# Performance work log

Hardware: AMD Instinct MI355X
Metric: run time of the kernel (lower is better)

## Reference

```python
import jax, jax.numpy as jnp
import numpy as np

H, NH, QLORA, KVLORA, DN, DR, DV = 2048, 16, 1536, 512, 128, 64, 128
QD = DN + DR  # 192
EPS = 1e-6
ROPE_BASE = 10000.0


def rmsnorm(x, g):
    var = jnp.mean(x * x, axis=-1, keepdims=True)
    return x * jax.lax.rsqrt(var + EPS) * g


def rotate_half(x):
    x1, x2 = jnp.split(x, 2, axis=-1)
    return jnp.concatenate([-x2, x1], axis=-1)


def rope_cos_sin(seq_len):
    inv_freq = 1.0 / (ROPE_BASE ** (jnp.arange(0, DR, 2, dtype=jnp.float32) / DR))
    t = jnp.arange(seq_len, dtype=jnp.float32)
    freqs = jnp.outer(t, inv_freq)           # [S, DR/2]
    emb = jnp.concatenate([freqs, freqs], -1)  # [S, DR]
    return jnp.cos(emb), jnp.sin(emb)


def setup_inputs() -> dict:
    key = jax.random.key(0)
    ks = jax.random.split(key, 6)
    B, S = 2, 2048
    sc = 0.02
    return {
        "hidden_states": jax.random.normal(ks[0], (B, S, H), jnp.float32),
        "w_qa": jax.random.normal(ks[1], (QLORA, H), jnp.float32) * sc,
        "g_qa": jnp.ones((QLORA,), jnp.float32),
        "w_qb": jax.random.normal(ks[2], (NH * QD, QLORA), jnp.float32) * sc,
        "w_kva": jax.random.normal(ks[3], (KVLORA + DR, H), jnp.float32) * sc,
        "g_kva": jnp.ones((KVLORA,), jnp.float32),
        "w_kvb": jax.random.normal(ks[4], (NH * (DN + DV), KVLORA), jnp.float32) * sc,
        "w_o": jax.random.normal(ks[5], (H, NH * DV), jnp.float32) * sc,
    }


def reference(hidden_states, w_qa, g_qa, w_qb, w_kva, g_kva, w_kvb, w_o):
    B, S, _ = hidden_states.shape
    # Q path: low-rank down-proj -> RMSNorm -> up-proj
    q_a = hidden_states @ w_qa.T                        # [B,S,QLORA]
    q = rmsnorm(q_a, g_qa) @ w_qb.T                     # [B,S,NH*QD]
    q = q.reshape(B, S, NH, QD).transpose(0, 2, 1, 3)   # [B,NH,S,QD]
    q_nope, q_pe = q[..., :DN], q[..., DN:]
    # KV path: joint down-proj with MQA rope slice
    ckv = hidden_states @ w_kva.T                       # [B,S,KVLORA+DR]
    compressed_kv, k_pe = ckv[..., :KVLORA], ckv[..., KVLORA:]
    k_pe = k_pe.reshape(B, S, 1, DR).transpose(0, 2, 1, 3)  # [B,1,S,DR]
    kv = rmsnorm(compressed_kv, g_kva) @ w_kvb.T        # [B,S,NH*(DN+DV)]
    kv = kv.reshape(B, S, NH, DN + DV).transpose(0, 2, 1, 3)
    k_nope, v = kv[..., :DN], kv[..., DN:]              # [B,NH,S,DN], [B,NH,S,DV]
    # decoupled RoPE on rope sub-dims only
    cos, sin = rope_cos_sin(S)                          # [S,DR]
    cos = cos[None, None]; sin = sin[None, None]
    q_pe = q_pe * cos + rotate_half(q_pe) * sin
    k_pe = k_pe * cos + rotate_half(k_pe) * sin
    query = jnp.concatenate([q_nope, q_pe], -1)         # [B,NH,S,QD]
    key = jnp.concatenate([k_nope, jnp.broadcast_to(k_pe, (B, NH, S, DR))], -1)
    # causal SDPA with scale = QD**-0.5
    scale = QD ** (-0.5)
    scores = jnp.einsum("bhsd,bhtd->bhst", query, key) * scale
    mask = jnp.tril(jnp.ones((S, S), bool))
    scores = jnp.where(mask, scores, jnp.finfo(scores.dtype).min)
    attn = jax.nn.softmax(scores, axis=-1)
    out = jnp.einsum("bhst,bhtd->bhsd", attn, v)        # [B,NH,S,DV]
    out = out.transpose(0, 2, 1, 3).reshape(B, S, NH * DV)
    return out @ w_o.T
```

## Files before the change

kernel.cpp:

```cpp
#include <hip/hip_runtime.h>
#include <cstdint>
#include <cstring>

typedef short short8 __attribute__((ext_vector_type(8)));
typedef float float4v __attribute__((ext_vector_type(4)));
typedef float float4g __attribute__((ext_vector_type(4)));
typedef unsigned short ushort4v __attribute__((ext_vector_type(4)));
typedef unsigned int uint2v __attribute__((ext_vector_type(2)));

typedef __attribute__((address_space(3))) unsigned int lds_uint;
typedef __attribute__((address_space(1))) const unsigned int glob_uint;

static __device__ __forceinline__ void async16(void* lds, const void* g) {
    __builtin_amdgcn_global_load_lds((glob_uint*)g, (lds_uint*)lds, 16, 0, 0);
}

static __device__ __forceinline__ float b2f(unsigned short u) {
    unsigned int x = ((unsigned int)u) << 16;
    float f;
    __builtin_memcpy(&f, &x, 4);
    return f;
}
static __device__ __forceinline__ unsigned short f2b(float f) {
    unsigned int x;
    __builtin_memcpy(&x, &f, 4);
    unsigned int r = (x + 0x7fffu + ((x >> 16) & 1u)) >> 16;
    return (unsigned short)r;
}

__global__ __launch_bounds__(256) void k_f2b6(
    const float* __restrict__ s0, unsigned short* __restrict__ d0,
    const float* __restrict__ s1, unsigned short* __restrict__ d1,
    const float* __restrict__ s2, unsigned short* __restrict__ d2,
    const float* __restrict__ s3, unsigned short* __restrict__ d3,
    const float* __restrict__ s4, unsigned short* __restrict__ d4,
    const float* __restrict__ s5, unsigned short* __restrict__ d5,
    float qs) {
    int blk = blockIdx.x;
    const float* s; unsigned short* d; float sc = 1.f; int rel;
    if (blk < 8192)       { s = s0; d = d0; rel = blk; }
    else if (blk < 11264) { s = s1; d = d1; rel = blk - 8192; }
    else if (blk < 15872) { s = s2; d = d2; rel = blk - 11264; sc = qs; }
    else if (blk < 17024) { s = s3; d = d3; rel = blk - 15872; }
    else if (blk < 19072) { s = s4; d = d4; rel = blk - 17024; }
    else                  { s = s5; d = d5; rel = blk - 19072; }
    int i = (rel * 256 + threadIdx.x) * 4;
    float4g v = *(const float4g*)(s + i);
    ushort4v r;
    r.x = f2b(v.x * sc); r.y = f2b(v.y * sc); r.z = f2b(v.z * sc); r.w = f2b(v.w * sc);
    *(ushort4v*)(d + i) = r;
}

static __device__ __forceinline__ void gemm_bt_body(
    const unsigned short* __restrict__ A, int lda,
    const unsigned short* __restrict__ W,
    void* __restrict__ C, int ldc,
    int N, int K, int mode, int bx, int by,
    unsigned short* __restrict__ VT) {
    __shared__ __align__(16) unsigned short As[128 * 32];
    __shared__ __align__(16) unsigned short Ws[128 * 32];
    const int tid = threadIdx.x;
    const int m0 = by * 128, n0 = bx * 128;
    const int wave = tid >> 6, lane = tid & 63;
    const int wm = (wave >> 1) * 64, wn = (wave & 1) * 64;
    const int lrow = lane & 15, quad = lane >> 4;
    const int srow = lane >> 2, spiece = lane & 3;

    float4v acc[4][4];
    float4v z = {0.f, 0.f, 0.f, 0.f};
#pragma unroll
    for (int i = 0; i < 4; i++)
#pragma unroll
        for (int j = 0; j < 4; j++) acc[i][j] = z;

    for (int k0 = 0; k0 < K; k0 += 32) {
#pragma unroll
        for (int ii = 0; ii < 2; ++ii) {
            int i = wave + ii * 4;
            int row = i * 16 + srow;
            async16(&As[i * 512], &A[(size_t)(m0 + row) * lda + k0 + spiece * 8]);
            int wr = n0 + row;
            if (wr > N - 1) wr = N - 1;
            async16(&Ws[i * 512], &W[(size_t)wr * K + k0 + spiece * 8]);
        }
        __syncthreads();
        short8 af[4], bfr[4];
#pragma unroll
        for (int i = 0; i < 4; i++)
            af[i] = *(const short8*)&As[(wm + i * 16 + lrow) * 32 + quad * 8];
#pragma unroll
        for (int i = 0; i < 4; i++)
            bfr[i] = *(const short8*)&Ws[(wn + i * 16 + lrow) * 32 + quad * 8];
#pragma unroll
        for (int i = 0; i < 4; i++)
#pragma unroll
            for (int j = 0; j < 4; j++)
                acc[i][j] = __builtin_amdgcn_mfma_f32_16x16x32_bf16(af[i], bfr[j], acc[i][j], 0, 0, 0);
        __syncthreads();
    }

    const int rbase = quad * 4;
#pragma unroll
    for (int i = 0; i < 4; i++) {
#pragma unroll
        for (int j = 0; j < 4; j++) {
            int col = n0 + wn + j * 16 + lrow;
            if (col >= N) continue;
            if (mode == 2) {
                int dd = col & 255, h = col >> 8;
                int row0 = m0 + wm + i * 16 + rbase;
                if (dd < 128) {
#pragma unroll
                    for (int r = 0; r < 4; r++)
                        ((unsigned short*)C)[(size_t)(row0 + r) * ldc + col] = f2b(acc[i][j][r]);
                } else {
                    int b = row0 >> 11, s0 = row0 & 2047;
                    ushort4v pv;
                    pv.x = f2b(acc[i][j][0]); pv.y = f2b(acc[i][j][1]);
                    pv.z = f2b(acc[i][j][2]); pv.w = f2b(acc[i][j][3]);
                    *(ushort4v*)&VT[((size_t)(b * 16 + h) * 128 + (dd - 128)) * 2048 + s0] = pv;
                }
            } else {
#pragma unroll
                for (int r = 0; r < 4; r++) {
                    int row = m0 + wm + i * 16 + rbase + r;
                    float v = acc[i][j][r];
                    if (mode == 1)
                        ((float*)C)[(size_t)row * ldc + col] = v;
                    else
                        ((unsigned short*)C)[(size_t)row * ldc + col] = f2b(v);
                }
            }
        }
    }
}

__global__ __launch_bounds__(256, 3)
void k_gemm_bt(const unsigned short* __restrict__ A, int lda,
               const unsigned short* __restrict__ W,
               void* __restrict__ C, int ldc,
               int N, int K, int mode) {
    gemm_bt_body(A, lda, W, C, ldc, N, K, mode, blockIdx.x, blockIdx.y, nullptr);
}

__global__ __launch_bounds__(256, 3)
void k_gemm_dual(const unsigned short* __restrict__ A0, int lda0,
                 const unsigned short* __restrict__ W0, void* __restrict__ C0,
                 int ldc0, int N0, int K0, int nbx0,
                 const unsigned short* __restrict__ A1, int lda1,
                 const unsigned short* __restrict__ W1, void* __restrict__ C1,
                 int ldc1, int N1, int K1, int mode1,
                 unsigned short* __restrict__ VT) {
    int bx = blockIdx.x;
    if (bx < nbx0) {
        gemm_bt_body(A0, lda0, W0, C0, ldc0, N0, K0, 0, bx, blockIdx.y, nullptr);
    } else {
        gemm_bt_body(A1, lda1, W1, C1, ldc1, N1, K1, mode1, bx - nbx0, blockIdx.y, VT);
    }
}

__global__ __launch_bounds__(192) void k_norm2(
    unsigned short* __restrict__ qa, const float* __restrict__ g_qa,
    unsigned short* __restrict__ ckv, const float* __restrict__ g_kva) {
    __shared__ float wsum[3];
    int blk = blockIdx.x;
    int tid = threadIdx.x;
    if (blk < 4096) {
        size_t base = (size_t)blk * 1536 + tid * 8;
        short8 v8 = *(const short8*)(qa + base);
        float vf[8];
        float ss = 0.f;
#pragma unroll
        for (int i = 0; i < 8; i++) {
            vf[i] = b2f((unsigned short)v8[i]);
            ss += vf[i] * vf[i];
        }
        for (int off = 32; off > 0; off >>= 1) ss += __shfl_xor(ss, off);
        int wave = tid >> 6, lane = tid & 63;
        if (lane == 0) wsum[wave] = ss;
        __syncthreads();
        ss = wsum[0] + wsum[1] + wsum[2];
        float scale = rsqrtf(ss * (1.f / 1536.f) + 1e-6f);
        short8 r8;
#pragma unroll
        for (int i = 0; i < 8; i++) r8[i] = (short)f2b(vf[i] * scale * g_qa[tid * 8 + i]);
        *(short8*)(qa + base) = r8;
    } else {
        int row = blk - 4096;
        if (tid < 64) {
            size_t base = (size_t)row * 576 + tid * 8;
            short8 v8 = *(const short8*)(ckv + base);
            float vf[8];
            float ss = 0.f;
#pragma unroll
            for (int i = 0; i < 8; i++) {
                vf[i] = b2f((unsigned short)v8[i]);
                ss += vf[i] * vf[i];
            }
            for (int off = 32; off > 0; off >>= 1) ss += __shfl_xor(ss, off);
            float scale = rsqrtf(ss * (1.f / 512.f) + 1e-6f);
            short8 r8;
#pragma unroll
            for (int i = 0; i < 8; i++) r8[i] = (short)f2b(vf[i] * scale * g_kva[tid * 8 + i]);
            *(short8*)(ckv + base) = r8;
        } else if (tid < 96) {
            int d = tid - 64;
            int s = row & 2047;
            size_t base = (size_t)row * 576 + 512;
            float inv = exp2f((float)d * -0.4152410118609203f);
            float f = (float)s * inv;
            float c, sn;
            sincosf(f, &sn, &c);
            float x1 = b2f(ckv[base + d]), x2 = b2f(ckv[base + d + 32]);
            ckv[base + d] = f2b(x1 * c - x2 * sn);
            ckv[base + d + 32] = f2b(x2 * c + x1 * sn);
        }
    }
}

__global__ __launch_bounds__(256, 2)
void k_attn11(const unsigned short* __restrict__ q,
              const unsigned short* __restrict__ kv,
              const unsigned short* __restrict__ ckv,
              const unsigned short* __restrict__ vt,
              unsigned short* __restrict__ ao)
{
    __shared__ __align__(16) unsigned short Ks[2][12288];
    __shared__ __align__(16) unsigned short Vs[8192];
    __shared__ __align__(16) unsigned short Pl[4][1280];

    const int lb = blockIdx.x;
    const int qt = (lb < 256) ? (lb >> 5) : 15 - ((lb & 255) >> 5);
    const int bh = lb & 31;
    const int b = bh >> 4, h = bh & 15;
    const int tid = threadIdx.x, wave = tid >> 6, lane = tid & 63;
    const int lrow = lane & 15, quad = lane >> 4;
    const int srow = lane >> 2, spiece = lane & 3;
    const int tok0 = b * 2048 + qt * 128;
    unsigned short* Pw = Pl[wave];

    const int colx = spiece ^ ((srow >> 1) & 3);
    const int qx = (quad ^ ((lrow >> 1) & 3)) * 8;

    short8 qf[2][6];
#pragma unroll
    for (int mi = 0; mi < 2; mi++) {
        int row = wave * 32 + mi * 16 + lrow;
        const unsigned short* qp = q + (size_t)(tok0 + row) * 3072 + h * 192;
#pragma unroll
        for (int ks = 0; ks < 6; ks++) qf[mi][ks] = *(const short8*)(qp + ks * 32 + quad * 8);
        float sp = (float)(qt * 128 + row);
#pragma unroll
        for (int j = 0; j < 8; j++) {
            float inv = exp2f((float)(quad * 8 + j) * -0.4152410118609203f);
            float f = sp * inv;
            float c, sn;
            sincosf(f, &sn, &c);
            float x1 = b2f((unsigned short)qf[mi][4][j]);
            float x2 = b2f((unsigned short)qf[mi][5][j]);
            qf[mi][4][j] = (short)f2b(x1 * c - x2 * sn);
            qf[mi][5][j] = (short)f2b(x2 * c + x1 * sn);
        }
    }

    short8 ones;
#pragma unroll
    for (int j = 0; j < 8; j++) ones[j] = (short)0x3F80;

    float m_st[2];
    m_st[0] = m_st[1] = -__builtin_inff();
    float4v z4 = {0.f, 0.f, 0.f, 0.f};
    float4v o[2][8], osum[2];
#pragma unroll
    for (int mi = 0; mi < 2; mi++) {
        osum[mi] = z4;
#pragma unroll
        for (int dt = 0; dt < 8; dt++) o[mi][dt] = z4;
    }

    const int nk = 2 * qt + 2;

    auto stageK = [&](int kt, int buf) {
        const int kb = kt * 64;
#pragma unroll
        for (int ii = 0; ii < 6; ++ii) {
            int id = wave * 6 + ii;
            int ks = id >> 2;
            int row = (id & 3) * 16 + srow;
            int key = b * 2048 + kb + row;
            const unsigned short* g =
                (ks < 4) ? kv + (size_t)key * 4096 + h * 256 + ks * 32 + colx * 8
                         : ckv + (size_t)key * 576 + 512 + (ks - 4) * 32 + colx * 8;
            async16(&Ks[buf][id * 512], g);
        }
    };
    auto stageV = [&](int kt) {
        const int kb = kt * 64;
#pragma unroll
        for (int ii = 0; ii < 4; ++ii) {
            int id = wave * 4 + ii;
            int d = (id & 7) * 16 + srow;
            const unsigned short* g =
                vt + ((size_t)bh * 128 + d) * 2048 + kb + (id >> 3) * 32 + colx * 8;
            async16(&Vs[id * 512], g);
        }
    };

    stageK(0, 0);

    for (int kt = 0; kt < nk; ++kt) {
        __syncthreads();
        stageV(kt);
        if (kt + 1 < nk) stageK(kt + 1, (kt + 1) & 1);
        const unsigned short* Kb = Ks[kt & 1];
        const int kb = kt * 64;

        float4v sc[2][4];
#pragma unroll
        for (int mi = 0; mi < 2; mi++)
#pragma unroll
            for (int nt = 0; nt < 4; nt++) sc[mi][nt] = z4;
        __builtin_amdgcn_s_setprio(1);
#pragma unroll
        for (int ks = 0; ks < 6; ks++) {
#pragma unroll
            for (int nt = 0; nt < 4; nt++) {
                short8 kf = *(const short8*)&Kb[ks * 2048 + nt * 512 + lrow * 32 + qx];
                sc[0][nt] = __builtin_amdgcn_mfma_f32_16x16x32_bf16(kf, qf[0][ks], sc[0][nt], 0, 0, 0);
                sc[1][nt] = __builtin_amdgcn_mfma_f32_16x16x32_bf16(kf, qf[1][ks], sc[1][nt], 0, 0, 0);
            }
        }
        __builtin_amdgcn_s_setprio(0);

        if (kt >= nk - 2) {
#pragma unroll
            for (int mi = 0; mi < 2; mi++) {
                int rowc = qt * 128 + wave * 32 + mi * 16 + lrow;
#pragma unroll
                for (int nt = 0; nt < 4; nt++)
#pragma unroll
                    for (int r = 0; r < 4; r++) {
                        int keyc = kb + nt * 16 + quad * 4 + r;
                        if (keyc > rowc) sc[mi][nt][r] = -__builtin_inff();
                    }
            }
        }

        float mx[2];
#pragma unroll
        for (int mi = 0; mi < 2; mi++) {
            float m = sc[mi][0][0];
#pragma unroll
            for (int nt = 0; nt < 4; nt++)
#pragma unroll
                for (int r = 0; r < 4; r++) m = fmaxf(m, sc[mi][nt][r]);
            m = fmaxf(m, __shfl_xor(m, 16));
            m = fmaxf(m, __shfl_xor(m, 32));
            mx[mi] = m;
        }
        bool within = (mx[0] <= m_st[0] + 6.f) && (mx[1] <= m_st[1] + 6.f);
        if (!__all(within)) {
            float alpha[2];
#pragma unroll
            for (int mi = 0; mi < 2; mi++) {
                float mnew = fmaxf(m_st[mi], mx[mi]);
                alpha[mi] = exp2f(m_st[mi] - mnew);
                m_st[mi] = mnew;
            }
            float arow[2][4];
#pragma unroll
            for (int mi = 0; mi < 2; mi++)
#pragma unroll
                for (int r = 0; r < 4; r++) arow[mi][r] = __shfl(alpha[mi], quad * 4 + r);
#pragma unroll
            for (int mi = 0; mi < 2; mi++) {
#pragma unroll
                for (int r = 0; r < 4; r++) osum[mi][r] *= arow[mi][r];
#pragma unroll
                for (int dt = 0; dt < 8; dt++)
#pragma unroll
                    for (int r = 0; r < 4; r++) o[mi][dt][r] *= arow[mi][r];
            }
        }
        uint2v pk[2][4];
#pragma unroll
        for (int mi = 0; mi < 2; mi++) {
#pragma unroll
            for (int nt = 0; nt < 4; nt++) {
                float p0 = exp2f(sc[mi][nt][0] - m_st[mi]);
                float p1 = exp2f(sc[mi][nt][1] - m_st[mi]);
                float p2 = exp2f(sc[mi][nt][2] - m_st[mi]);
                float p3 = exp2f(sc[mi][nt][3] - m_st[mi]);
                pk[mi][nt].x = (unsigned int)f2b(p0) | ((unsigned int)f2b(p1) << 16);
                pk[mi][nt].y = (unsigned int)f2b(p2) | ((unsigned int)f2b(p3) << 16);
            }
        }

        __syncthreads();

#pragma unroll
        for (int ks2 = 0; ks2 < 2; ks2++) {
#pragma unroll
            for (int mi = 0; mi < 2; mi++) {
                int row = mi * 16 + lrow;
                *(uint2v*)&Pw[row * 40 + quad * 4] = pk[mi][ks2 * 2];
                *(uint2v*)&Pw[row * 40 + 16 + quad * 4] = pk[mi][ks2 * 2 + 1];
            }
            short8 pa0 = *(const short8*)&Pw[lrow * 40 + quad * 8];
            short8 pa1 = *(const short8*)&Pw[(16 + lrow) * 40 + quad * 8];
            __builtin_amdgcn_s_setprio(1);
#pragma unroll
            for (int dt = 0; dt < 8; dt++) {
                short8 vf = *(const short8*)&Vs[(ks2 * 8 + dt) * 512 + lrow * 32 + qx];
                o[0][dt] = __builtin_amdgcn_mfma_f32_16x16x32_bf16(pa0, vf, o[0][dt], 0, 0, 0);
                o[1][dt] = __builtin_amdgcn_mfma_f32_16x16x32_bf16(pa1, vf, o[1][dt], 0, 0, 0);
            }
            osum[0] = __builtin_amdgcn_mfma_f32_16x16x32_bf16(pa0, ones, osum[0], 0, 0, 0);
            osum[1] = __builtin_amdgcn_mfma_f32_16x16x32_bf16(pa1, ones, osum[1], 0, 0, 0);
            __builtin_amdgcn_s_setprio(0);
        }
    }

#pragma unroll
    for (int mi = 0; mi < 2; mi++) {
#pragma unroll
        for (int r = 0; r < 4; r++) {
            float linv = 1.f / osum[mi][r];
            unsigned short* dst =
                ao + (size_t)(tok0 + wave * 32 + mi * 16 + quad * 4 + r) * 2048 + h * 128;
#pragma unroll
            for (int dt = 0; dt < 8; dt++) dst[dt * 16 + lrow] = f2b(o[mi][dt][r] * linv);
        }
    }
}

extern "C" void kernel_launch(void* const* d_in, const int* in_sizes, int n_in,
                              void* d_out, int out_size, void* d_ws, size_t ws_size,
                              hipStream_t stream) {
    (void)in_sizes; (void)n_in; (void)out_size; (void)ws_size;
    const float* hs    = (const float*)d_in[0];
    const float* w_qa  = (const float*)d_in[1];
    const float* g_qa  = (const float*)d_in[2];
    const float* w_qb  = (const float*)d_in[3];
    const float* w_kva = (const float*)d_in[4];
    const float* g_kva = (const float*)d_in[5];
    const float* w_kvb = (const float*)d_in[6];
    const float* w_o   = (const float*)d_in[7];

    char* ws = (char*)d_ws;
    size_t off = 0;
    auto alloc = [&](size_t bytes) -> unsigned short* {
        unsigned short* p = (unsigned short*)(ws + off);
        off += (bytes + 255) & ~(size_t)255;
        return p;
    };
    unsigned short* hb    = alloc(4096ull * 2048 * 2);
    unsigned short* wqa   = alloc(1536ull * 2048 * 2);
    unsigned short* wqb   = alloc(3072ull * 1536 * 2);
    unsigned short* wkva  = alloc(576ull * 2048 * 2);
    unsigned short* wkvb  = alloc(4096ull * 512 * 2);
    unsigned short* wo    = alloc(2048ull * 2048 * 2);
    unsigned short* qa    = alloc(4096ull * 1536 * 2);
    unsigned short* ckv   = alloc(4096ull * 576 * 2);
    unsigned short* qbuf  = alloc(4096ull * 3072 * 2);
    unsigned short* kvbuf = alloc(4096ull * 4096 * 2);
    unsigned short* vtb   = alloc(32ull * 128 * 2048 * 2);
    unsigned short* ao    = alloc(4096ull * 2048 * 2);

    const float qscale = 0.07216878364870323f * 1.4426950408889634f;

    k_f2b6<<<dim3(23168), dim3(256), 0, stream>>>(
        hs, hb, w_qa, wqa, w_qb, wqb, w_kva, wkva, w_kvb, wkvb, w_o, wo, qscale);

    k_gemm_dual<<<dim3(17, 32), 256, 0, stream>>>(
        hb, 2048, wqa, qa, 1536, 1536, 2048, 12,
        hb, 2048, wkva, ckv, 576, 576, 2048, 0, nullptr);

    k_norm2<<<dim3(8192), dim3(192), 0, stream>>>(qa, g_qa, ckv, g_kva);

    k_gemm_dual<<<dim3(56, 32), 256, 0, stream>>>(
        qa, 1536, wqb, qbuf, 3072, 3072, 1536, 24,
        ckv, 576, wkvb, kvbuf, 4096, 4096, 512, 2, vtb);

    k_attn11<<<dim3(512), 256, 0, stream>>>(qbuf, kvbuf, ckv, vtb, ao);
    k_gemm_bt<<<dim3(16, 32), 256, 0, stream>>>(ao, 2048, wo, d_out, 2048, 2048, 2048, 1);
}
```

Measured before the change: 432.6 us.

## Triple-buffer GEMM LDS tiles with async prefetch two stages ahead

Replaces the single-buffered LDS tile loop in the shared GEMM body with a 3-stage ring buffer. Global-to-LDS async loads for tile t+2 are issued before the MFMA work on tile t, and explicit vmcnt waits plus barriers replace the two __syncthreads per iteration. The aim is to hide global load latency behind matrix math and cut barrier stalls. In exchange LDS use triples, which can lower occupancy, and correctness depends on the hand-written vmcnt counts.

Measured after the change: 447.1 us. 3.3% more time.

```diff
diff --git a/kernel.cpp b/kernel.cpp
--- a/kernel.cpp
+++ b/kernel.cpp
@@ -57,8 +57,8 @@
     void* __restrict__ C, int ldc,
     int N, int K, int mode, int bx, int by,
     unsigned short* __restrict__ VT) {
-    __shared__ __align__(16) unsigned short As[128 * 32];
-    __shared__ __align__(16) unsigned short Ws[128 * 32];
+    __shared__ __align__(16) unsigned short As[3][128 * 32];
+    __shared__ __align__(16) unsigned short Ws[3][128 * 32];
     const int tid = threadIdx.x;
     const int m0 = by * 128, n0 = bx * 128;
     const int wave = tid >> 6, lane = tid & 63;
@@ -66,37 +66,57 @@
     const int lrow = lane & 15, quad = lane >> 4;
     const int srow = lane >> 2, spiece = lane & 3;
 
-    float4v acc[4][4];
-    float4v z = {0.f, 0.f, 0.f, 0.f};
-#pragma unroll
-    for (int i = 0; i < 4; i++)
-#pragma unroll
-        for (int j = 0; j < 4; j++) acc[i][j] = z;
-
-    for (int k0 = 0; k0 < K; k0 += 32) {
+    auto stage = [&](int t, int buf) {
+        const int k0 = t * 32;
 #pragma unroll
         for (int ii = 0; ii < 2; ++ii) {
             int i = wave + ii * 4;
             int row = i * 16 + srow;
-            async16(&As[i * 512], &A[(size_t)(m0 + row) * lda + k0 + spiece * 8]);
+            async16(&As[buf][i * 512], &A[(size_t)(m0 + row) * lda + k0 + spiece * 8]);
             int wr = n0 + row;
             if (wr > N - 1) wr = N - 1;
-            async16(&Ws[i * 512], &W[(size_t)wr * K + k0 + spiece * 8]);
-        }
-        __syncthreads();
+            async16(&Ws[buf][i * 512], &W[(size_t)wr * K + k0 + spiece * 8]);
+        }
+    };
+
+    float4v acc[4][4];
+    float4v z = {0.f, 0.f, 0.f, 0.f};
+#pragma unroll
+    for (int i = 0; i < 4; i++)
+#pragma unroll
+        for (int j = 0; j < 4; j++) acc[i][j] = z;
+
+    const int nt = K >> 5;
+
+    stage(0, 0);
+    stage(1, 1);
+    asm volatile("s_waitcnt vmcnt(4)" ::: "memory");
+    __builtin_amdgcn_s_barrier();
+
+    for (int t = 0; t < nt; ++t) {
+        const int cur = t % 3;
+        if (t + 2 < nt) stage(t + 2, (t + 2) % 3);
+
         short8 af[4], bfr[4];
 #pragma unroll
         for (int i = 0; i < 4; i++)
-            af[i] = *(const short8*)&As[(wm + i * 16 + lrow) * 32 + quad * 8];
+            af[i] = *(const short8*)&As[cur][(wm + i * 16 + lrow) * 32 + quad * 8];
 #pragma unroll
         for (int i = 0; i < 4; i++)
-            bfr[i] = *(const short8*)&Ws[(wn + i * 16 + lrow) * 32 + quad * 8];
+            bfr[i] = *(const short8*)&Ws[cur][(wn + i * 16 + lrow) * 32 + quad * 8];
 #pragma unroll
         for (int i = 0; i < 4; i++)
 #pragma unroll
             for (int j = 0; j < 4; j++)
                 acc[i][j] = __builtin_amdgcn_mfma_f32_16x16x32_bf16(af[i], bfr[j], acc[i][j], 0, 0, 0);
-        __syncthreads();
+
+        if (t + 2 < nt) {
+            asm volatile("s_waitcnt vmcnt(4)" ::: "memory");
+            __builtin_amdgcn_s_barrier();
+        } else if (t + 1 < nt) {
+            asm volatile("s_waitcnt vmcnt(0)" ::: "memory");
+            __builtin_amdgcn_s_barrier();
+        }
     }
 
     const int rbase = quad * 4;
```

## Use 256x256-tile 512-thread GEMM for the Q/KV up-projection

Applied to the files above, without the earlier changes.

Adds a new GEMM body with 256x256 output tiles, 8 waves per block, a double-buffered async LDS staging of 64-wide K slices with XOR swizzle, and prefetch split across four compute phases. It replaces the 128-tile dual GEMM for the q_b and kv_b up-projections. Larger tiles raise arithmetic intensity and cut redundant global loads of A and W. In exchange there are fewer blocks (448) and heavy LDS (128KB) and register use, which lowers occupancy and may cause a wave-quantization tail.

Measured after the change: 464.0 us. 7.2% more time.

```diff
diff --git a/kernel.cpp b/kernel.cpp
--- a/kernel.cpp
+++ b/kernel.cpp
@@ -159,6 +159,138 @@
     }
 }
 
+static __device__ __forceinline__ void gemm256_body(
+    const unsigned short* __restrict__ A, int lda,
+    const unsigned short* __restrict__ W,
+    void* __restrict__ C, int ldc,
+    int N, int K, int mode, int bx, int by,
+    unsigned short* __restrict__ VT) {
+    __shared__ __align__(16) unsigned short Ab[2][256 * 64];
+    __shared__ __align__(16) unsigned short Bb[2][256 * 64];
+    const int tid = threadIdx.x;
+    const int m0 = by * 256, n0 = bx * 256;
+    const int wave = tid >> 6, lane = tid & 63;
+    const int wm = (wave >> 2) * 128, wn = (wave & 3) * 64;
+    const int lrow = lane & 15, quad = lane >> 4;
+
+    int srow_[4], scol_[4];
+#pragma unroll
+    for (int l = 0; l < 4; l++) {
+        int c = l * 512 + tid;
+        srow_[l] = c >> 3;
+        scol_[l] = (c & 7) ^ ((c >> 3) & 7);
+    }
+    auto stageA = [&](int t, int buf, int l) {
+        int c = l * 512 + tid;
+        async16(&Ab[buf][c * 8], &A[(size_t)(m0 + srow_[l]) * lda + t * 64 + scol_[l] * 8]);
+    };
+    auto stageB = [&](int t, int buf, int l) {
+        int c = l * 512 + tid;
+        int wr = n0 + srow_[l];
+        if (wr > N - 1) wr = N - 1;
+        async16(&Bb[buf][c * 8], &W[(size_t)wr * K + t * 64 + scol_[l] * 8]);
+    };
+
+    float4v acc[8][4];
+    float4v z = {0.f, 0.f, 0.f, 0.f};
+#pragma unroll
+    for (int i = 0; i < 8; i++)
+#pragma unroll
+        for (int j = 0; j < 4; j++) acc[i][j] = z;
+
+    const int nt = K >> 6;
+
+#pragma unroll
+    for (int l = 0; l < 4; l++) { stageA(0, 0, l); stageB(0, 0, l); }
+    __syncthreads();
+
+    for (int t = 0; t < nt; ++t) {
+        const int cur = t & 1;
+#pragma unroll
+        for (int ph = 0; ph < 4; ++ph) {
+            const int mq = ph >> 1, nq = ph & 1;
+            if (t + 1 < nt) { stageA(t + 1, cur ^ 1, ph); stageB(t + 1, cur ^ 1, ph); }
+            short8 af[4][2], bf[2][2];
+#pragma unroll
+            for (int kk = 0; kk < 2; kk++) {
+                const int sl = ((kk * 4 + quad) ^ (lrow & 7)) * 8;
+#pragma unroll
+                for (int i = 0; i < 4; i++) {
+                    int row = wm + mq * 64 + i * 16 + lrow;
+                    af[i][kk] = *(const short8*)&Ab[cur][row * 64 + sl];
+                }
+#pragma unroll
+                for (int j = 0; j < 2; j++) {
+                    int col = wn + nq * 32 + j * 16 + lrow;
+                    bf[j][kk] = *(const short8*)&Bb[cur][col * 64 + sl];
+                }
+            }
+            __builtin_amdgcn_s_setprio(1);
+#pragma unroll
+            for (int i = 0; i < 4; i++)
+#pragma unroll
+                for (int j = 0; j < 2; j++) {
+                    int ai = mq * 4 + i, bj = nq * 2 + j;
+                    acc[ai][bj] = __builtin_amdgcn_mfma_f32_16x16x32_bf16(af[i][0], bf[j][0], acc[ai][bj], 0, 0, 0);
+                    acc[ai][bj] = __builtin_amdgcn_mfma_f32_16x16x32_bf16(af[i][1], bf[j][1], acc[ai][bj], 0, 0, 0);
+                }
+            __builtin_amdgcn_s_setprio(0);
+        }
+        __syncthreads();
+    }
+
+    const int rbase = quad * 4;
+#pragma unroll
+    for (int ai = 0; ai < 8; ai++) {
+#pragma unroll
+        for (int bj = 0; bj < 4; bj++) {
+            int col = n0 + wn + bj * 16 + lrow;
+            if (col >= N) continue;
+            if (mode == 2) {
+                int dd = col & 255, h = col >> 8;
+                int row0 = m0 + wm + ai * 16 + rbase;
+                if (dd < 128) {
+#pragma unroll
+                    for (int r = 0; r < 4; r++)
+                        ((unsigned short*)C)[(size_t)(row0 + r) * ldc + col] = f2b(acc[ai][bj][r]);
+                } else {
+                    int b = row0 >> 11, s0 = row0 & 2047;
+                    ushort4v pv;
+                    pv.x = f2b(acc[ai][bj][0]); pv.y = f2b(acc[ai][bj][1]);
+                    pv.z = f2b(acc[ai][bj][2]); pv.w = f2b(acc[ai][bj][3]);
+                    *(ushort4v*)&VT[((size_t)(b * 16 + h) * 128 + (dd - 128)) * 2048 + s0] = pv;
+                }
+            } else {
+#pragma unroll
+                for (int r = 0; r < 4; r++) {
+                    int row = m0 + wm + ai * 16 + rbase + r;
+                    float v = acc[ai][bj][r];
+                    if (mode == 1)
+                        ((float*)C)[(size_t)row * ldc + col] = v;
+                    else
+                        ((unsigned short*)C)[(size_t)row * ldc + col] = f2b(v);
+                }
+            }
+        }
+    }
+}
+
+__global__ __launch_bounds__(512, 2)
+void k_gemm256_dual(const unsigned short* __restrict__ A0, int lda0,
+                    const unsigned short* __restrict__ W0, void* __restrict__ C0,
+                    int ldc0, int N0, int K0, int nbx0,
+                    const unsigned short* __restrict__ A1, int lda1,
+                    const unsigned short* __restrict__ W1, void* __restrict__ C1,
+                    int ldc1, int N1, int K1, int mode1,
+                    unsigned short* __restrict__ VT) {
+    int bx = blockIdx.x;
+    if (bx < nbx0) {
+        gemm256_body(A0, lda0, W0, C0, ldc0, N0, K0, 0, bx, blockIdx.y, nullptr);
+    } else {
+        gemm256_body(A1, lda1, W1, C1, ldc1, N1, K1, mode1, bx - nbx0, blockIdx.y, VT);
+    }
+}
+
 __global__ __launch_bounds__(192) void k_norm2(
     unsigned short* __restrict__ qa, const float* __restrict__ g_qa,
     unsigned short* __restrict__ ckv, const float* __restrict__ g_kva) {
@@ -478,8 +610,8 @@
 
     k_norm2<<<dim3(8192), dim3(192), 0, stream>>>(qa, g_qa, ckv, g_kva);
 
-    k_gemm_dual<<<dim3(56, 32), 256, 0, stream>>>(
-        qa, 1536, wqb, qbuf, 3072, 3072, 1536, 24,
+    k_gemm256_dual<<<dim3(28, 16), 512, 0, stream>>>(
+        qa, 1536, wqb, qbuf, 3072, 3072, 1536, 12,
         ckv, 576, wkvb, kvbuf, 4096, 4096, 512, 2, vtb);
 
     k_attn11<<<dim3(512), 256, 0, stream>>>(qbuf, kvbuf, ckv, vtb, ao);
```
